# Performance work log

Measured on AMD Instinct MI355X. Metric: run time of the kernel, lower is better.

The kernel has to match this reference:

```python
import jax, jax.numpy as jnp
import numpy as np

B, S, HID = 32, 577, 768
NH, HD = 12, 64  # num heads, head dim (HID = NH*HD)


def setup_inputs() -> dict:
    key = jax.random.key(0)
    ks = jax.random.split(key, 8)
    scale = 1.0 / np.sqrt(HID)
    return {
        "hidden_states": jax.random.normal(ks[0], (B, S, HID), jnp.float32),
        "lateral_states": jax.random.normal(ks[1], (B, NH, S, HD), jnp.float32),
        "Wq": jax.random.normal(ks[2], (HID, HID), jnp.float32) * scale,
        "bq": jax.random.normal(ks[3], (HID,), jnp.float32) * 0.02,
        "Wk": jax.random.normal(ks[4], (HID, HID), jnp.float32) * scale,
        "bk": jax.random.normal(ks[5], (HID,), jnp.float32) * 0.02,
        "Wv": jax.random.normal(ks[6], (HID, HID), jnp.float32) * scale,
        "bv": jax.random.normal(ks[7], (HID,), jnp.float32) * 0.02,
        "mix_with": 0,  # 0 -> 'q', 1 -> 'k', 2 -> 'v'
    }


def _heads(x):
    # [B, S, HID] -> [B, NH, S, HD]
    return x.reshape(B, S, NH, HD).transpose(0, 2, 1, 3)


def reference(hidden_states, lateral_states, Wq, bq, Wk, bk, Wv, bv, mix_with):
    q = _heads(hidden_states @ Wq.T + bq)
    k = _heads(hidden_states @ Wk.T + bk)
    v = _heads(hidden_states @ Wv.T + bv)
    if mix_with == 0:
        q = q * lateral_states
    elif mix_with == 1:
        k = k * lateral_states
    elif mix_with == 2:
        v = v * lateral_states
    else:
        raise ValueError("mix_with must be 0 (q), 1 (k), or 2 (v)")
    scores = jnp.einsum("bhqd,bhkd->bhqk", q, k) / jnp.sqrt(jnp.float32(HD))
    probs = jax.nn.softmax(scores, axis=-1)
    ctx = jnp.einsum("bhqk,bhkd->bhqd", probs, v)
    # [B, NH, S, HD] -> [B, S, HID]
    return ctx.transpose(0, 2, 1, 3).reshape(B, S, HID)
```

## Files before the change

kernel.cpp:

```cpp
#include <hip/hip_runtime.h>

#define B_    32
#define S_    577
#define HID_  768
#define NH_   12
#define HD_   64
#define SPAD  640
#define SB_   5
#define MT_   160
#define KT_   12
#define NT_   18

typedef __attribute__((ext_vector_type(8))) short short8;
typedef __attribute__((ext_vector_type(4))) short short4s;
typedef __attribute__((ext_vector_type(4))) float float4_;

static __device__ __forceinline__ float bf2f(short s) {
    union { float f; unsigned u; } cvt;
    cvt.u = ((unsigned)(unsigned short)s) << 16;
    return cvt.f;
}
static __device__ __forceinline__ short f2bf(float f) {
    union { float f; unsigned u; } cvt;
    cvt.f = f;
    unsigned u = cvt.u;
    unsigned r = u + 0x7FFF + ((u >> 16) & 1);
    return (short)(r >> 16);
}

__global__ __launch_bounds__(256) void convA_kernel(
    const float* __restrict__ X, short* __restrict__ ximg)
{
    const int mt = blockIdx.x, kt = blockIdx.y;
    const int b = mt / SB_, sb = mt - b * SB_;
    short* img = ximg + ((size_t)mt * KT_ + kt) * 8192;
#pragma unroll
    for (int i = 0; i < 4; ++i) {
        const int j = i * 256 + threadIdx.x;
        const int row = j >> 3, kg = j & 7;
        const int s = sb * 128 + row;
        const int srow = (s < S_) ? s : 0;
        const float* src = X + ((size_t)b * S_ + srow) * HID_ + kt * 64 + kg * 8;
        float4_ f0 = *(const float4_*)src;
        float4_ f1 = *(const float4_*)(src + 4);
        short8 s8;
#pragma unroll
        for (int e = 0; e < 4; ++e) { s8[e] = f2bf(f0[e]); s8[e + 4] = f2bf(f1[e]); }
        *(short8*)(img + ((size_t)kg * 128 + row) * 8) = s8;
    }
}

__global__ __launch_bounds__(256) void convB_kernel(
    const float* __restrict__ Wq, const float* __restrict__ Wk,
    const float* __restrict__ Wv, short* __restrict__ wimg)
{
    const int nt = blockIdx.x, kt = blockIdx.y;
    const int z = nt / 6;
    const float* W = (z == 0) ? Wq : (z == 1) ? Wk : Wv;
    const int n0 = (nt - z * 6) * 128;
    short* img = wimg + ((size_t)nt * KT_ + kt) * 8192;
#pragma unroll
    for (int i = 0; i < 4; ++i) {
        const int j = i * 256 + threadIdx.x;
        const int row = j >> 3, kg = j & 7;
        const float* src = W + (size_t)(n0 + row) * HID_ + kt * 64 + kg * 8;
        float4_ f0 = *(const float4_*)src;
        float4_ f1 = *(const float4_*)(src + 4);
        short8 s8;
#pragma unroll
        for (int e = 0; e < 4; ++e) { s8[e] = f2bf(f0[e]); s8[e + 4] = f2bf(f1[e]); }
        *(short8*)(img + ((size_t)kg * 128 + row) * 8) = s8;
    }
}

__global__ __launch_bounds__(256) void gemm_kernel(
    const short* __restrict__ ximg, const short* __restrict__ wimg,
    const float* __restrict__ bq, const float* __restrict__ bk,
    const float* __restrict__ bv,
    const float* __restrict__ lat, const int* __restrict__ mixw,
    short* __restrict__ qo, short* __restrict__ ko, short* __restrict__ vo)
{
    __shared__ __align__(16) short eP[4][4608];

    const int bid0 = blockIdx.x;
    const int bids = (bid0 & 7) * 360 + (bid0 >> 3);
    const int mt = bids / NT_;
    const int nt = bids - mt * NT_;

    const int z   = nt / 6;
    const int nz0 = (nt - z * 6) * 128;
    const int b   = mt / SB_;
    const int s0  = (mt - b * SB_) * 128;

    const int tid  = threadIdx.x;
    const int wave = tid >> 6;
    const int lane = tid & 63;
    const int quad = lane >> 4;
    const int l16  = lane & 15;

    const short* ag = ximg + ((size_t)mt * KT_) * 8192;
    const short* bg = wimg + ((size_t)nt * KT_) * 8192;

    float4_ acc[4][4] = {};
    const int r0 = (wave & 1) * 64 + l16;
    const int c0 = (wave >> 1) * 64 + l16;

    for (int kt = 0; kt < KT_; ++kt) {
        const short* ak = ag + (size_t)kt * 8192;
        const short* bk8p = bg + (size_t)kt * 8192;
#pragma unroll
        for (int c = 0; c < 2; ++c) {
            const int kb = (c * 4 + quad) * 128;
            short8 af[4], bf4[4];
#pragma unroll
            for (int mi = 0; mi < 4; ++mi)
                af[mi] = *(const short8*)(ak + (kb + r0 + mi * 16) * 8);
#pragma unroll
            for (int g = 0; g < 4; ++g)
                bf4[g] = *(const short8*)(bk8p + (kb + c0 + g * 16) * 8);
            __builtin_amdgcn_s_setprio(1);
#pragma unroll
            for (int mi = 0; mi < 4; ++mi)
#pragma unroll
                for (int g = 0; g < 4; ++g)
                    acc[mi][g] = __builtin_amdgcn_mfma_f32_16x16x32_bf16(
                        af[mi], bf4[g], acc[mi][g], 0, 0, 0);
            __builtin_amdgcn_s_setprio(0);
        }
    }

    const int mwv = *mixw;
    const float* bb = (z == 0) ? bq : (z == 1) ? bk : bv;
    const int hh   = (nz0 + (wave >> 1) * 64) >> 6;
    const size_t bh = (size_t)b * NH_ + hh;
    const int sW   = s0 + (wave & 1) * 64;
    const int ch   = sW >> 6;
    short* P = eP[wave];

    if (z < 2) {
#pragma unroll
        for (int mi = 0; mi < 4; ++mi)
#pragma unroll
            for (int i = 0; i < 4; ++i) {
                const int ml = mi * 16 + quad * 4 + i;
                const int s  = sW + ml;
                const float* lp =
                    lat + (bh * S_ + (s < S_ ? s : S_ - 1)) * HD_;
#pragma unroll
                for (int g = 0; g < 4; ++g) {
                    const int d = g * 16 + l16;
                    float val = acc[mi][g][i] + bb[hh * 64 + d];
                    if (z == mwv) val *= lp[d];
                    P[ml * 72 + d] = f2bf(val);
                }
            }
    } else {
#pragma unroll
        for (int mi = 0; mi < 4; ++mi)
#pragma unroll
            for (int g = 0; g < 4; ++g) {
                const int d  = g * 16 + l16;
                const int mb = mi * 16 + quad * 4;
                short4s w;
#pragma unroll
                for (int i = 0; i < 4; ++i) {
                    const int s = sW + mb + i;
                    float val = acc[mi][g][i] + bb[hh * 64 + d];
                    if (mwv == 2)
                        val *= lat[(bh * S_ + (s < S_ ? s : S_ - 1)) * HD_ + d];
                    w[i] = f2bf(val);
                }
                *(short4s*)(P + d * 72 + mb) = w;
            }
    }

    const int rr = lane >> 3, cc = lane & 7;
    if (z == 0) {
        short* qb = qo + (size_t)bh * SPAD * HD_;
#pragma unroll
        for (int j = 0; j < 8; ++j) {
            const int r = j * 8 + rr;
            *(short8*)(qb + (size_t)(sW + r) * 64 + cc * 8) =
                *(const short8*)(P + r * 72 + cc * 8);
        }
    } else if (z == 1) {
        short* kb_ = ko + ((size_t)bh * 10 + ch) * 4096;
#pragma unroll
        for (int j = 0; j < 8; ++j) {
            const int r = j * 8 + rr;
            *(short8*)(kb_ + (cc * 64 + r) * 8) =
                *(const short8*)(P + r * 72 + cc * 8);
        }
    } else {
        short* vb = vo + ((size_t)bh * 10 + ch) * 4096;
#pragma unroll
        for (int j = 0; j < 8; ++j) {
            const int r = j * 8 + rr;
            *(short8*)(vb + (cc * 64 + r) * 8) =
                *(const short8*)(P + r * 72 + cc * 8);
        }
    }
}

__global__ __launch_bounds__(256) void attn_kernel(
    const short* __restrict__ q, const short* __restrict__ k,
    const short* __restrict__ vt, float* __restrict__ out)
{
    __shared__ __align__(16) short pbuf[4][16][64];

    const int bid0 = blockIdx.x;
    const int bids = (bid0 & 7) * 480 + (bid0 >> 3);
    const int bh = bids / 10;
    const int qt = bids - bh * 10;

    const int b    = bh / NH_;
    const int h    = bh - b * NH_;
    const int tid  = threadIdx.x;
    const int wave = tid >> 6;
    const int lane = tid & 63;
    const int quad = lane >> 4;
    const int l16  = lane & 15;
    const int q0   = qt * 64 + wave * 16;

    const short* qp   = q  + (size_t)bh * SPAD * HD_;
    const short* kimg = k  + (size_t)bh * 40960;
    const short* vimg = vt + (size_t)bh * 40960;

    const short8 aq0 = *(const short8*)(qp + (size_t)(q0 + l16) * HD_ + quad * 8);
    const short8 aq1 = *(const short8*)(qp + (size_t)(q0 + l16) * HD_ + 32 + quad * 8);

    float m_i = -3.0e38f, l_i = 0.0f;
    float4_ O[4] = {};

    char* pw = (char*)&pbuf[wave][l16][0];
    const int swz = (l16 & 7) << 4;

    for (int kc = 0; kc < 10; ++kc) {
        const short* Kc = kimg + (size_t)kc * 4096;
        const short* Vc = vimg + (size_t)kc * 4096;

        float4_ sc[4] = {};
#pragma unroll
        for (int c = 0; c < 2; ++c) {
            const int kb = (c * 4 + quad) * 64;
            const short8 aq = c ? aq1 : aq0;
            short8 kf[4];
#pragma unroll
            for (int g = 0; g < 4; ++g)
                kf[g] = *(const short8*)(Kc + (kb + g * 16 + l16) * 8);
            __builtin_amdgcn_s_setprio(1);
#pragma unroll
            for (int g = 0; g < 4; ++g)
                sc[g] = __builtin_amdgcn_mfma_f32_16x16x32_bf16(kf[g], aq, sc[g], 0, 0, 0);
            __builtin_amdgcn_s_setprio(0);
        }

        if (kc == 9) {
#pragma unroll
            for (int g = 0; g < 4; ++g)
#pragma unroll
                for (int i = 0; i < 4; ++i)
                    if (576 + g * 16 + quad * 4 + i >= S_) sc[g][i] = -3.0e38f;
        }

        float cm = sc[0][0];
#pragma unroll
        for (int g = 0; g < 4; ++g)
#pragma unroll
            for (int i = 0; i < 4; ++i) cm = fmaxf(cm, sc[g][i]);
        cm = fmaxf(cm, __shfl_xor(cm, 16));
        cm = fmaxf(cm, __shfl_xor(cm, 32));

        const float mn    = fmaxf(m_i, cm);
        const float alpha = __expf((m_i - mn) * 0.125f);
        m_i = mn;
        const float mo = mn * 0.125f;

        float rs = 0.0f;
#pragma unroll
        for (int g = 0; g < 4; ++g) {
            short4s w;
#pragma unroll
            for (int i = 0; i < 4; ++i) {
                const float p = __expf(__builtin_fmaf(sc[g][i], 0.125f, -mo));
                const short pb = f2bf(p);
                w[i] = pb;
                rs += bf2f(pb);
            }
            *(short4s*)(pw + ((g * 32 + quad * 8) ^ swz)) = w;
        }
        rs += __shfl_xor(rs, 16);
        rs += __shfl_xor(rs, 32);
        l_i = l_i * alpha + rs;

        float av[4];
#pragma unroll
        for (int i = 0; i < 4; ++i)
            av[i] = __shfl(alpha, quad * 20 + i);
#pragma unroll
        for (int g = 0; g < 4; ++g)
#pragma unroll
            for (int i = 0; i < 4; ++i) O[g][i] *= av[i];

#pragma unroll
        for (int c = 0; c < 2; ++c) {
            const short8 ap =
                *(const short8*)(pw + ((c * 64 + quad * 16) ^ swz));
            const int kb = (c * 4 + quad) * 64;
            short8 vf[4];
#pragma unroll
            for (int g = 0; g < 4; ++g)
                vf[g] = *(const short8*)(Vc + (kb + g * 16 + l16) * 8);
            __builtin_amdgcn_s_setprio(1);
#pragma unroll
            for (int g = 0; g < 4; ++g)
                O[g] = __builtin_amdgcn_mfma_f32_16x16x32_bf16(ap, vf[g], O[g], 0, 0, 0);
            __builtin_amdgcn_s_setprio(0);
        }
    }

    float linv[4];
#pragma unroll
    for (int i = 0; i < 4; ++i)
        linv[i] = 1.0f / __shfl(l_i, quad * 20 + i);
#pragma unroll
    for (int i = 0; i < 4; ++i) {
        const int s = q0 + quad * 4 + i;
        if (s >= S_) continue;
#pragma unroll
        for (int g = 0; g < 4; ++g)
            out[((size_t)b * S_ + s) * HID_ + h * HD_ + g * 16 + l16] =
                O[g][i] * linv[i];
    }
}

extern "C" void kernel_launch(void* const* d_in, const int* in_sizes, int n_in,
                              void* d_out, int out_size, void* d_ws, size_t ws_size,
                              hipStream_t stream) {
    (void)in_sizes; (void)n_in; (void)out_size; (void)ws_size;

    const float* X   = (const float*)d_in[0];
    const float* lat = (const float*)d_in[1];
    const float* Wq  = (const float*)d_in[2];
    const float* bq  = (const float*)d_in[3];
    const float* Wk  = (const float*)d_in[4];
    const float* bk  = (const float*)d_in[5];
    const float* Wv  = (const float*)d_in[6];
    const float* bv  = (const float*)d_in[7];
    const int* mixw  = (const int*)d_in[8];
    float* out = (float*)d_out;

    const size_t per = (size_t)B_ * NH_ * SPAD * HD_;
    short* qw   = (short*)d_ws;
    short* kw   = qw + per;
    short* vw   = kw + per;
    short* wimg = vw + per;
    short* ximg = wimg + (size_t)NT_ * KT_ * 8192;

    convA_kernel<<<dim3(MT_, KT_), 256, 0, stream>>>(X, ximg);
    convB_kernel<<<dim3(NT_, KT_), 256, 0, stream>>>(Wq, Wk, Wv, wimg);
    gemm_kernel<<<dim3(2880), 256, 0, stream>>>(
        ximg, wimg, bq, bk, bv, lat, mixw, qw, kw, vw);
    attn_kernel<<<dim3(3840), 256, 0, stream>>>(qw, kw, vw, out);
}
```

Baseline: 386.9 us.

## Software-pipeline global loads in GEMM and attention loops, add nontemporal memory hints

The GEMM main loop becomes a three-stage register pipeline: fragments for the next k-phases are loaded while MFMAs run on the current set, and the loop is fully unrolled through macros. The attention loop double-buffers K fragments across chunks and issues V loads before the QK MFMAs so global latency overlaps compute. Many loads and stores across the conversion, GEMM epilogue and attention output become nontemporal to reduce cache pollution. The extra register buffers raise VGPR pressure and may cut occupancy. Nontemporal stores to the q/k/v intermediates that the next kernel rereads could also cost cache hits.

```diff
diff --git a/kernel.cpp b/kernel.cpp
--- a/kernel.cpp
+++ b/kernel.cpp
@@ -41,12 +41,12 @@
         const int s = sb * 128 + row;
         const int srow = (s < S_) ? s : 0;
         const float* src = X + ((size_t)b * S_ + srow) * HID_ + kt * 64 + kg * 8;
-        float4_ f0 = *(const float4_*)src;
-        float4_ f1 = *(const float4_*)(src + 4);
+        float4_ f0 = __builtin_nontemporal_load((const float4_*)src);
+        float4_ f1 = __builtin_nontemporal_load((const float4_*)(src + 4));
         short8 s8;
 #pragma unroll
         for (int e = 0; e < 4; ++e) { s8[e] = f2bf(f0[e]); s8[e + 4] = f2bf(f1[e]); }
-        *(short8*)(img + ((size_t)kg * 128 + row) * 8) = s8;
+        __builtin_nontemporal_store(s8, (short8*)(img + ((size_t)kg * 128 + row) * 8));
     }
 }
 
@@ -64,13 +64,36 @@
         const int j = i * 256 + threadIdx.x;
         const int row = j >> 3, kg = j & 7;
         const float* src = W + (size_t)(n0 + row) * HID_ + kt * 64 + kg * 8;
-        float4_ f0 = *(const float4_*)src;
-        float4_ f1 = *(const float4_*)(src + 4);
+        float4_ f0 = __builtin_nontemporal_load((const float4_*)src);
+        float4_ f1 = __builtin_nontemporal_load((const float4_*)(src + 4));
         short8 s8;
 #pragma unroll
         for (int e = 0; e < 4; ++e) { s8[e] = f2bf(f0[e]); s8[e + 4] = f2bf(f1[e]); }
-        *(short8*)(img + ((size_t)kg * 128 + row) * 8) = s8;
-    }
+        __builtin_nontemporal_store(s8, (short8*)(img + ((size_t)kg * 128 + row) * 8));
+    }
+}
+
+#define LOADSET(S, PH) {                                                      \
+    const int _p = (PH);                                                      \
+    const short* _ak = ag + (size_t)(_p >> 1) * 8192;                         \
+    const short* _bk = bg + (size_t)(_p >> 1) * 8192;                         \
+    const int _kb = ((_p & 1) * 4 + quad) * 128;                              \
+    _Pragma("unroll")                                                         \
+    for (int mi = 0; mi < 4; ++mi)                                            \
+        S##a[mi] = *(const short8*)(_ak + (_kb + r0 + mi * 16) * 8);          \
+    _Pragma("unroll")                                                         \
+    for (int g = 0; g < 4; ++g)                                               \
+        S##b[g] = *(const short8*)(_bk + (_kb + c0 + g * 16) * 8);            \
+}
+#define MFMASET(S) {                                                          \
+    __builtin_amdgcn_s_setprio(1);                                            \
+    _Pragma("unroll")                                                         \
+    for (int mi = 0; mi < 4; ++mi)                                            \
+        _Pragma("unroll")                                                     \
+        for (int g = 0; g < 4; ++g)                                           \
+            acc[mi][g] = __builtin_amdgcn_mfma_f32_16x16x32_bf16(             \
+                S##a[mi], S##b[g], acc[mi][g], 0, 0, 0);                      \
+    __builtin_amdgcn_s_setprio(0);                                            \
 }
 
 __global__ __launch_bounds__(256) void gemm_kernel(
@@ -105,28 +128,18 @@
     const int r0 = (wave & 1) * 64 + l16;
     const int c0 = (wave >> 1) * 64 + l16;
 
-    for (int kt = 0; kt < KT_; ++kt) {
-        const short* ak = ag + (size_t)kt * 8192;
-        const short* bk8p = bg + (size_t)kt * 8192;
-#pragma unroll
-        for (int c = 0; c < 2; ++c) {
-            const int kb = (c * 4 + quad) * 128;
-            short8 af[4], bf4[4];
-#pragma unroll
-            for (int mi = 0; mi < 4; ++mi)
-                af[mi] = *(const short8*)(ak + (kb + r0 + mi * 16) * 8);
-#pragma unroll
-            for (int g = 0; g < 4; ++g)
-                bf4[g] = *(const short8*)(bk8p + (kb + c0 + g * 16) * 8);
-            __builtin_amdgcn_s_setprio(1);
-#pragma unroll
-            for (int mi = 0; mi < 4; ++mi)
-#pragma unroll
-                for (int g = 0; g < 4; ++g)
-                    acc[mi][g] = __builtin_amdgcn_mfma_f32_16x16x32_bf16(
-                        af[mi], bf4[g], acc[mi][g], 0, 0, 0);
-            __builtin_amdgcn_s_setprio(0);
-        }
+    short8 Aa[4], Ab[4], Ba[4], Bb[4], Ca[4], Cb[4];
+
+    LOADSET(A, 0);
+    LOADSET(B, 1);
+    for (int it = 0; it < 4; ++it) {
+        const int p = it * 6;
+        LOADSET(C, p + 2);                       MFMASET(A);
+        LOADSET(A, p + 3);                       MFMASET(B);
+        LOADSET(B, p + 4);                       MFMASET(C);
+        LOADSET(C, p + 5);                       MFMASET(A);
+        LOADSET(A, (p + 6 < 24) ? p + 6 : 0);    MFMASET(B);
+        LOADSET(B, (p + 7 < 24) ? p + 7 : 1);    MFMASET(C);
     }
 
     const int mwv = *mixw;
@@ -150,7 +163,7 @@
                 for (int g = 0; g < 4; ++g) {
                     const int d = g * 16 + l16;
                     float val = acc[mi][g][i] + bb[hh * 64 + d];
-                    if (z == mwv) val *= lp[d];
+                    if (z == mwv) val *= __builtin_nontemporal_load(lp + d);
                     P[ml * 72 + d] = f2bf(val);
                 }
             }
@@ -167,7 +180,8 @@
                     const int s = sW + mb + i;
                     float val = acc[mi][g][i] + bb[hh * 64 + d];
                     if (mwv == 2)
-                        val *= lat[(bh * S_ + (s < S_ ? s : S_ - 1)) * HD_ + d];
+                        val *= __builtin_nontemporal_load(
+                            lat + (bh * S_ + (s < S_ ? s : S_ - 1)) * HD_ + d);
                     w[i] = f2bf(val);
                 }
                 *(short4s*)(P + d * 72 + mb) = w;
@@ -180,26 +194,109 @@
 #pragma unroll
         for (int j = 0; j < 8; ++j) {
             const int r = j * 8 + rr;
-            *(short8*)(qb + (size_t)(sW + r) * 64 + cc * 8) =
-                *(const short8*)(P + r * 72 + cc * 8);
+            __builtin_nontemporal_store(
+                *(const short8*)(P + r * 72 + cc * 8),
+                (short8*)(qb + (size_t)(sW + r) * 64 + cc * 8));
         }
     } else if (z == 1) {
         short* kb_ = ko + ((size_t)bh * 10 + ch) * 4096;
 #pragma unroll
         for (int j = 0; j < 8; ++j) {
             const int r = j * 8 + rr;
-            *(short8*)(kb_ + (cc * 64 + r) * 8) =
-                *(const short8*)(P + r * 72 + cc * 8);
+            __builtin_nontemporal_store(
+                *(const short8*)(P + r * 72 + cc * 8),
+                (short8*)(kb_ + (cc * 64 + r) * 8));
         }
     } else {
         short* vb = vo + ((size_t)bh * 10 + ch) * 4096;
 #pragma unroll
         for (int j = 0; j < 8; ++j) {
             const int r = j * 8 + rr;
-            *(short8*)(vb + (cc * 64 + r) * 8) =
-                *(const short8*)(P + r * 72 + cc * 8);
+            __builtin_nontemporal_store(
+                *(const short8*)(P + r * 72 + cc * 8),
+                (short8*)(vb + (cc * 64 + r) * 8));
         }
     }
+}
+
+#define ATTN_CHUNK(KC, KCUR, KNXT) {                                          \
+    const int _kc = (KC);                                                     \
+    const short* Vc = vimg + (size_t)_kc * 4096;                              \
+    short8 vf[2][4];                                                          \
+    _Pragma("unroll")                                                         \
+    for (int c = 0; c < 2; ++c)                                               \
+        _Pragma("unroll")                                                     \
+        for (int g = 0; g < 4; ++g)                                           \
+            vf[c][g] = *(const short8*)(Vc + (((c*4+quad)*64) + g*16 + l16)*8);\
+    float4_ sc[4] = {};                                                       \
+    __builtin_amdgcn_s_setprio(1);                                            \
+    _Pragma("unroll")                                                         \
+    for (int c = 0; c < 2; ++c)                                               \
+        _Pragma("unroll")                                                     \
+        for (int g = 0; g < 4; ++g)                                           \
+            sc[g] = __builtin_amdgcn_mfma_f32_16x16x32_bf16(                  \
+                KCUR[c][g], c ? aq1 : aq0, sc[g], 0, 0, 0);                   \
+    __builtin_amdgcn_s_setprio(0);                                            \
+    {   const int _kn = (_kc == 9) ? 0 : _kc + 1;                             \
+        const short* Kn = kimg + (size_t)_kn * 4096;                          \
+        _Pragma("unroll")                                                     \
+        for (int c = 0; c < 2; ++c)                                           \
+            _Pragma("unroll")                                                 \
+            for (int g = 0; g < 4; ++g)                                       \
+                KNXT[c][g] = *(const short8*)                                 \
+                    (Kn + (((c*4+quad)*64) + g*16 + l16)*8);                  \
+    }                                                                         \
+    if (_kc == 9) {                                                           \
+        _Pragma("unroll")                                                     \
+        for (int g = 0; g < 4; ++g)                                           \
+            _Pragma("unroll")                                                 \
+            for (int i = 0; i < 4; ++i)                                       \
+                if (576 + g * 16 + quad * 4 + i >= S_) sc[g][i] = -3.0e38f;   \
+    }                                                                         \
+    float cm = sc[0][0];                                                      \
+    _Pragma("unroll")                                                         \
+    for (int g = 0; g < 4; ++g)                                               \
+        _Pragma("unroll")                                                     \
+        for (int i = 0; i < 4; ++i) cm = fmaxf(cm, sc[g][i]);                 \
+    cm = fmaxf(cm, __shfl_xor(cm, 16));                                       \
+    cm = fmaxf(cm, __shfl_xor(cm, 32));                                       \
+    const float mn    = fmaxf(m_i, cm);                                       \
+    const float alpha = __expf((m_i - mn) * 0.125f);                          \
+    m_i = mn;                                                                 \
+    const float mo = mn * 0.125f;                                             \
+    float rs = 0.0f;                                                          \
+    _Pragma("unroll")                                                         \
+    for (int g = 0; g < 4; ++g) {                                             \
+        short4s w;                                                            \
+        _Pragma("unroll")                                                     \
+        for (int i = 0; i < 4; ++i) {                                         \
+            const float p = __expf(__builtin_fmaf(sc[g][i], 0.125f, -mo));    \
+            const short pb = f2bf(p);                                         \
+            w[i] = pb;                                                        \
+            rs += bf2f(pb);                                                   \
+        }                                                                     \
+        *(short4s*)(pw + ((g * 32 + quad * 8) ^ swz)) = w;                    \
+    }                                                                         \
+    rs += __shfl_xor(rs, 16);                                                 \
+    rs += __shfl_xor(rs, 32);                                                 \
+    l_i = l_i * alpha + rs;                                                   \
+    float av[4];                                                              \
+    _Pragma("unroll")                                                         \
+    for (int i = 0; i < 4; ++i) av[i] = __shfl(alpha, quad * 20 + i);         \
+    _Pragma("unroll")                                                         \
+    for (int g = 0; g < 4; ++g)                                               \
+        _Pragma("unroll")                                                     \
+        for (int i = 0; i < 4; ++i) O[g][i] *= av[i];                         \
+    _Pragma("unroll")                                                         \
+    for (int c = 0; c < 2; ++c) {                                             \
+        const short8 ap = *(const short8*)(pw + ((c * 64 + quad * 16) ^ swz));\
+        __builtin_amdgcn_s_setprio(1);                                        \
+        _Pragma("unroll")                                                     \
+        for (int g = 0; g < 4; ++g)                                           \
+            O[g] = __builtin_amdgcn_mfma_f32_16x16x32_bf16(                   \
+                ap, vf[c][g], O[g], 0, 0, 0);                                 \
+        __builtin_amdgcn_s_setprio(0);                                        \
+    }                                                                         \
 }
 
 __global__ __launch_bounds__(256) void attn_kernel(
@@ -226,8 +323,10 @@
     const short* kimg = k  + (size_t)bh * 40960;
     const short* vimg = vt + (size_t)bh * 40960;
 
-    const short8 aq0 = *(const short8*)(qp + (size_t)(q0 + l16) * HD_ + quad * 8);
-    const short8 aq1 = *(const short8*)(qp + (size_t)(q0 + l16) * HD_ + 32 + quad * 8);
+    const short8 aq0 = __builtin_nontemporal_load(
+        (const short8*)(qp + (size_t)(q0 + l16) * HD_ + quad * 8));
+    const short8 aq1 = __builtin_nontemporal_load(
+        (const short8*)(qp + (size_t)(q0 + l16) * HD_ + 32 + quad * 8));
 
     float m_i = -3.0e38f, l_i = 0.0f;
     float4_ O[4] = {};
@@ -235,88 +334,16 @@
     char* pw = (char*)&pbuf[wave][l16][0];
     const int swz = (l16 & 7) << 4;
 
-    for (int kc = 0; kc < 10; ++kc) {
-        const short* Kc = kimg + (size_t)kc * 4096;
-        const short* Vc = vimg + (size_t)kc * 4096;
-
-        float4_ sc[4] = {};
-#pragma unroll
-        for (int c = 0; c < 2; ++c) {
-            const int kb = (c * 4 + quad) * 64;
-            const short8 aq = c ? aq1 : aq0;
-            short8 kf[4];
-#pragma unroll
-            for (int g = 0; g < 4; ++g)
-                kf[g] = *(const short8*)(Kc + (kb + g * 16 + l16) * 8);
-            __builtin_amdgcn_s_setprio(1);
-#pragma unroll
-            for (int g = 0; g < 4; ++g)
-                sc[g] = __builtin_amdgcn_mfma_f32_16x16x32_bf16(kf[g], aq, sc[g], 0, 0, 0);
-            __builtin_amdgcn_s_setprio(0);
-        }
-
-        if (kc == 9) {
-#pragma unroll
-            for (int g = 0; g < 4; ++g)
-#pragma unroll
-                for (int i = 0; i < 4; ++i)
-                    if (576 + g * 16 + quad * 4 + i >= S_) sc[g][i] = -3.0e38f;
-        }
-
-        float cm = sc[0][0];
+    short8 kfA[2][4], kfB[2][4];
+#pragma unroll
+    for (int c = 0; c < 2; ++c)
 #pragma unroll
         for (int g = 0; g < 4; ++g)
-#pragma unroll
-            for (int i = 0; i < 4; ++i) cm = fmaxf(cm, sc[g][i]);
-        cm = fmaxf(cm, __shfl_xor(cm, 16));
-        cm = fmaxf(cm, __shfl_xor(cm, 32));
-
-        const float mn    = fmaxf(m_i, cm);
-        const float alpha = __expf((m_i - mn) * 0.125f);
-        m_i = mn;
-        const float mo = mn * 0.125f;
-
-        float rs = 0.0f;
-#pragma unroll
-        for (int g = 0; g < 4; ++g) {
-            short4s w;
-#pragma unroll
-            for (int i = 0; i < 4; ++i) {
-                const float p = __expf(__builtin_fmaf(sc[g][i], 0.125f, -mo));
-                const short pb = f2bf(p);
-                w[i] = pb;
-                rs += bf2f(pb);
-            }
-            *(short4s*)(pw + ((g * 32 + quad * 8) ^ swz)) = w;
-        }
-        rs += __shfl_xor(rs, 16);
-        rs += __shfl_xor(rs, 32);
-        l_i = l_i * alpha + rs;
-
-        float av[4];
-#pragma unroll
-        for (int i = 0; i < 4; ++i)
-            av[i] = __shfl(alpha, quad * 20 + i);
-#pragma unroll
-        for (int g = 0; g < 4; ++g)
-#pragma unroll
-            for (int i = 0; i < 4; ++i) O[g][i] *= av[i];
-
-#pragma unroll
-        for (int c = 0; c < 2; ++c) {
-            const short8 ap =
-                *(const short8*)(pw + ((c * 64 + quad * 16) ^ swz));
-            const int kb = (c * 4 + quad) * 64;
-            short8 vf[4];
-#pragma unroll
-            for (int g = 0; g < 4; ++g)
-                vf[g] = *(const short8*)(Vc + (kb + g * 16 + l16) * 8);
-            __builtin_amdgcn_s_setprio(1);
-#pragma unroll
-            for (int g = 0; g < 4; ++g)
-                O[g] = __builtin_amdgcn_mfma_f32_16x16x32_bf16(ap, vf[g], O[g], 0, 0, 0);
-            __builtin_amdgcn_s_setprio(0);
-        }
+            kfA[c][g] = *(const short8*)(kimg + (((c*4+quad)*64) + g*16 + l16)*8);
+
+    for (int kc2 = 0; kc2 < 10; kc2 += 2) {
+        ATTN_CHUNK(kc2,     kfA, kfB);
+        ATTN_CHUNK(kc2 + 1, kfB, kfA);
     }
 
     float linv[4];
@@ -329,8 +356,9 @@
         if (s >= S_) continue;
 #pragma unroll
         for (int g = 0; g < 4; ++g)
-            out[((size_t)b * S_ + s) * HID_ + h * HD_ + g * 16 + l16] =
-                O[g][i] * linv[i];
+            __builtin_nontemporal_store(
+                O[g][i] * linv[i],
+                out + ((size_t)b * S_ + s) * HID_ + h * HD_ + g * 16 + l16);
     }
 }
 
```

Result: slower. 419.0 us (+8.3%).
